# Kernel optimization log

Measured on AMD Instinct MI355X. Metric: run time of the kernel, lower is better.

The kernel has to match this reference:

```python
import jax, jax.numpy as jnp
import numpy as np

N, C, H = 8192, 512, 8


def setup_inputs() -> dict:
    key = jax.random.key(0)
    ks = jax.random.split(key, 5)
    s = 1.0 / np.sqrt(C)
    return {
        "x": jax.random.normal(ks[0], (N, C), dtype=jnp.float32),
        "W_theta": jax.random.normal(ks[1], (C, C), dtype=jnp.float32) * s,
        "b_theta": jnp.zeros((C,), dtype=jnp.float32),
        "W_phi": jax.random.normal(ks[2], (C, C), dtype=jnp.float32) * s,
        "b_phi": jnp.zeros((C,), dtype=jnp.float32),
        "W_k": jax.random.normal(ks[3], (H, C, C), dtype=jnp.float32) * s,
        "b_k": jnp.zeros((H, C), dtype=jnp.float32),
    }


def reference(x, W_theta, b_theta, W_phi, b_phi, W_k, b_k):
    # query/key projections: (N, C)
    query = x @ W_theta + b_theta
    key = x @ W_phi + b_phi
    # dense N x N similarity + row softmax
    sim = query @ key.T                       # (N, N)
    adj = jax.nn.softmax(sim, axis=-1)        # (N, N)
    # per-head V projections, batched: (H, N, C)
    xk = jnp.einsum("nc,hcd->hnd", x, W_k) + b_k[:, None, :]
    # attention-weighted aggregation per head, relu, mean over heads
    out = jnp.einsum("nm,hmd->hnd", adj, xk)  # (H, N, C)
    return jax.nn.relu(out).mean(axis=0)      # (N, C)
```

## Files before the change

### kernel.cpp

```cpp
#include <hip/hip_runtime.h>
#include <hip/hip_bf16.h>
#include <cstdint>
#include <cstddef>

#define NN 8192
#define CC 512
#define HH 8

typedef __attribute__((ext_vector_type(8))) short short8;
typedef __attribute__((ext_vector_type(4))) float f32x4;

__device__ __forceinline__ void gload_lds16(const void* g, void* l) {
  __builtin_amdgcn_global_load_lds(
      (const __attribute__((address_space(1))) void*)g,
      (__attribute__((address_space(3))) void*)l, 16, 0, 0);
}

__device__ __forceinline__ f32x4 mfma16(short8 a, short8 b, f32x4 c) {
  return __builtin_amdgcn_mfma_f32_16x16x32_bf16(a, b, c, 0, 0, 0);
}

__device__ __forceinline__ float b2f(unsigned u) {
  union { unsigned i; float f; } x; x.i = u << 16; return x.f;
}

__device__ __forceinline__ void unpack8(uint4 v, float* f) {
  f[0] = b2f(v.x & 0xffffu); f[1] = b2f(v.x >> 16);
  f[2] = b2f(v.y & 0xffffu); f[3] = b2f(v.y >> 16);
  f[4] = b2f(v.z & 0xffffu); f[5] = b2f(v.z >> 16);
  f[6] = b2f(v.w & 0xffffu); f[7] = b2f(v.w >> 16);
}

__global__ __launch_bounds__(256, 2) void gemm_qk(
    const __hip_bfloat16* __restrict__ ah, const __hip_bfloat16* __restrict__ al, int lda,
    const __hip_bfloat16* __restrict__ bh, const __hip_bfloat16* __restrict__ bl, int ldb,
    int K,
    __hip_bfloat16* __restrict__ outHi, __hip_bfloat16* __restrict__ outLo, int ldc,
    const float* __restrict__ biasCol)
{
  __shared__ __align__(16) char lds[32768];
  const int tid  = threadIdx.x;
  const int lane = tid & 63;
  const int wave = tid >> 6;
  const int bm = blockIdx.y, bn = blockIdx.x;
  const int wr = wave >> 1, wc = wave & 1;
  const int fr = lane & 15, fq = lane >> 4;

  f32x4 acc[4][4] = {};

  for (int kt = 0; kt < K; kt += 32) {
    __syncthreads();
#pragma unroll
    for (int tile = 0; tile < 4; ++tile) {
      const __hip_bfloat16* tp = (tile == 0) ? ah : (tile == 1) ? al
                               : (tile == 2) ? bh : bl;
      const int ld = (tile < 2) ? lda : ldb;
      const int tb = ((tile < 2) ? bm : bn) * 128;
#pragma unroll
      for (int half = 0; half < 2; ++half) {
        int sub = half * 256 + tid;
        int row = sub >> 2, ch = sub & 3;
        gload_lds16(tp + (size_t)(tb + row) * ld + kt + ch * 8,
                    lds + tile * 8192 + sub * 16);
      }
    }
    __syncthreads();

    short8 fah[4], fal[4], fbh[4], fbl[4];
#pragma unroll
    for (int i = 0; i < 4; ++i) {
      const int ra = (wr * 64 + i * 16 + fr) * 64 + fq * 16;
      const int rb = (wc * 64 + i * 16 + fr) * 64 + fq * 16;
      fah[i] = *(const short8*)(lds +         ra);
      fal[i] = *(const short8*)(lds +  8192 + ra);
      fbh[i] = *(const short8*)(lds + 16384 + rb);
      fbl[i] = *(const short8*)(lds + 24576 + rb);
    }
#pragma unroll
    for (int i = 0; i < 4; ++i)
#pragma unroll
      for (int j = 0; j < 4; ++j) {
        acc[i][j] = mfma16(fah[i], fbh[j], acc[i][j]);
        acc[i][j] = mfma16(fah[i], fbl[j], acc[i][j]);
        acc[i][j] = mfma16(fal[i], fbh[j], acc[i][j]);
      }
  }

#pragma unroll
  for (int i = 0; i < 4; ++i)
#pragma unroll
    for (int j = 0; j < 4; ++j) {
      const int rbase = bm * 128 + wr * 64 + i * 16 + fq * 4;
      const int col   = bn * 128 + wc * 64 + j * 16 + fr;
#pragma unroll
      for (int t = 0; t < 4; ++t) {
        float v = acc[i][j][t] + biasCol[col];
        __hip_bfloat16 h = __float2bfloat16(v);
        outHi[(size_t)(rbase + t) * ldc + col] = h;
        outLo[(size_t)(rbase + t) * ldc + col] = __float2bfloat16(v - __bfloat162float(h));
      }
    }
}

__global__ __launch_bounds__(512, 2) void gemm_sim(
    const __hip_bfloat16* __restrict__ A, int lda,
    const __hip_bfloat16* __restrict__ B, int ldb,
    int K,
    float* __restrict__ segMax, unsigned char* __restrict__ sim4)
{
  (void)K;
  __shared__ __align__(16) char lds[98304];
  const int tid  = threadIdx.x;
  const int lane = tid & 63;
  const int wave = tid >> 6;
  const int bm = blockIdx.y, bn = blockIdx.x;
  const int wm = wave >> 2;
  const int wn = wave & 3;
  const int fr = lane & 15, fq = lane >> 4;

  int s0 = tid * 16;          s0 ^= ((s0 >> 9) & 1) << 5;
  int s1 = 8192 + tid * 16;   s1 ^= ((s1 >> 9) & 1) << 5;
  const int off0 = (s0 >> 6) * 1024 + ((s0 & 63) >> 1);
  const int off1 = (s1 >> 6) * 1024 + ((s1 & 63) >> 1);

  const int fl = ((fr >> 3) & 1) << 5;
  const int baseAs = (((wm * 128 + fr) * 64) + fq * 16) ^ fl;
  const int baseBs = (((wn * 64 + fr) * 64) + fq * 16) ^ fl;

  const __hip_bfloat16* Ab = A + (size_t)bm * 256 * lda;
  const __hip_bfloat16* Bb = B + (size_t)bn * 256 * ldb;

#define STAGE_C0(t, buf) do {                                                \
    const __hip_bfloat16* ap_ = Ab + (t) * 32;                               \
    const __hip_bfloat16* bp_ = Bb + (t) * 32;                               \
    gload_lds16(ap_ + off0, lds + (buf) * 16384 + tid * 16);                 \
    gload_lds16(bp_ + off0, lds + 49152 + (buf) * 16384 + tid * 16);         \
  } while (0)
#define STAGE_C1(t, buf) do {                                                \
    const __hip_bfloat16* ap_ = Ab + (t) * 32;                               \
    const __hip_bfloat16* bp_ = Bb + (t) * 32;                               \
    gload_lds16(ap_ + off1, lds + (buf) * 16384 + 8192 + tid * 16);          \
    gload_lds16(bp_ + off1, lds + 49152 + (buf) * 16384 + 8192 + tid * 16);  \
  } while (0)

  f32x4 acc[8][4] = {};

  STAGE_C0(0, 0); STAGE_C1(0, 0);
  STAGE_C0(1, 1); STAGE_C1(1, 1);

#pragma unroll
  for (int t = 0; t < 16; ++t) {
    const int buf = t % 3;
    const int nbuf = (t + 2) % 3;
    const char* Abuf = lds + buf * 16384;
    const char* Bbuf = lds + 49152 + buf * 16384;

    if (t == 15) asm volatile("s_waitcnt vmcnt(0)" ::: "memory");
    else         asm volatile("s_waitcnt vmcnt(4)" ::: "memory");
    __builtin_amdgcn_s_barrier();
    __builtin_amdgcn_sched_barrier(0);

    short8 a[8], b4[4];
#pragma unroll
    for (int i = 0; i < 4; ++i)
      a[i] = *(const short8*)(Abuf + baseAs + i * 1024);
#pragma unroll
    for (int j = 0; j < 4; ++j)
      b4[j] = *(const short8*)(Bbuf + baseBs + j * 1024);
    if (t < 14) STAGE_C0(t + 2, nbuf);

#pragma unroll
    for (int i = 0; i < 4; ++i)
#pragma unroll
      for (int j = 0; j < 4; ++j)
        acc[i][j] = mfma16(a[i], b4[j], acc[i][j]);

#pragma unroll
    for (int i = 0; i < 4; ++i)
      a[4 + i] = *(const short8*)(Abuf + baseAs + (4 + i) * 1024);
    if (t < 14) STAGE_C1(t + 2, nbuf);

#pragma unroll
    for (int i = 0; i < 4; ++i)
#pragma unroll
      for (int j = 0; j < 4; ++j)
        acc[4 + i][j] = mfma16(a[4 + i], b4[j], acc[4 + i][j]);
  }
#undef STAGE_C0
#undef STAGE_C1

  const int seg = bn * 4 + wn;
#pragma unroll
  for (int i = 0; i < 8; ++i)
#pragma unroll
    for (int tt = 0; tt < 4; ++tt) {
      const int row = bm * 256 + wm * 128 + i * 16 + fq * 4 + tt;
      float mx = fmaxf(fmaxf(acc[i][0][tt], acc[i][1][tt]),
                       fmaxf(acc[i][2][tt], acc[i][3][tt]));
      mx = fmaxf(mx, __shfl_xor(mx, 1));
      mx = fmaxf(mx, __shfl_xor(mx, 2));
      mx = fmaxf(mx, __shfl_xor(mx, 4));
      mx = fmaxf(mx, __shfl_xor(mx, 8));
      if (fr == 0) segMax[(size_t)row * 128 + seg] = mx;
      unsigned q[4];
#pragma unroll
      for (int j = 0; j < 4; ++j)
        q[j] = (unsigned)fminf((mx - acc[i][j][tt]) * (4.0f / 3.0f), 15.0f);
      unsigned char* dst = sim4 + (size_t)row * (NN / 2) + seg * 32 + fr;
      dst[0]  = (unsigned char)(q[0] | (q[1] << 4));
      dst[16] = (unsigned char)(q[2] | (q[3] << 4));
    }
}

__global__ __launch_bounds__(256) void select_zgather(
    const float* __restrict__ segMax, const unsigned char* __restrict__ sim4,
    const __hip_bfloat16* __restrict__ QKhi, const __hip_bfloat16* __restrict__ QKlo,
    const float* __restrict__ x,
    __hip_bfloat16* __restrict__ z)
{
  const int lane = threadIdx.x & 63;
  const int n = blockIdx.x * 4 + (threadIdx.x >> 6);

  float2 sm = ((const float2*)(segMax + (size_t)n * 128))[lane];
  float M = fmaxf(sm.x, sm.y);
#pragma unroll
  for (int off = 32; off; off >>= 1) M = fmaxf(M, __shfl_xor(M, off));

  const unsigned long long b0 = __ballot(sm.x > M - 11.0f);
  const unsigned long long b1 = __ballot(sm.y > M - 11.0f);

  float qf[8];
  {
    uint4 qh4 = ((const uint4*)(QKhi + (size_t)n * 1024))[lane];
    uint4 ql4 = ((const uint4*)(QKlo + (size_t)n * 1024))[lane];
    float a[8], b[8];
    unpack8(qh4, a); unpack8(ql4, b);
#pragma unroll
    for (int e = 0; e < 8; ++e) qf[e] = a[e] + b[e];
  }

  const unsigned char* srow4 = sim4 + (size_t)n * (NN / 2);
  const int jj = lane >> 4;
  const int shift = (jj & 1) * 4;
  const int boff = (jj >> 1) * 16 + (lane & 15);

  int nk = 0;
  float se_mine = -1e30f;
  int   mm_mine = 0;
#pragma unroll
  for (int half = 0; half < 2; ++half) {
    unsigned long long mask = half ? b1 : b0;
    while (mask) {
      const int b = __ffsll((unsigned long long)mask) - 1;
      mask &= mask - 1;
      const int seg = 2 * b + half;
      const float segv = __shfl(half ? sm.y : sm.x, b);
      const unsigned byte = srow4[seg * 32 + boff];
      const float sa = segv - 0.75f * (float)((byte >> shift) & 15u);
      unsigned long long cm = __ballot(sa > M - 11.0f);
      while (cm) {
        const int c = __ffsll((unsigned long long)cm) - 1;
        cm &= cm - 1;
        const int m = seg * 64 + c;
        uint4 kh4 = ((const uint4*)(QKhi + (size_t)m * 1024 + 512))[lane];
        uint4 kl4 = ((const uint4*)(QKlo + (size_t)m * 1024 + 512))[lane];
        float a[8], bb[8];
        unpack8(kh4, a); unpack8(kl4, bb);
        float p = 0.f;
#pragma unroll
        for (int e = 0; e < 8; ++e) p += qf[e] * (a[e] + bb[e]);
#pragma unroll
        for (int off = 32; off; off >>= 1) p += __shfl_xor(p, off);
        if (p > M - 10.5f) {
          if (lane == nk) { se_mine = p; mm_mine = m; }
          nk = (nk < 63) ? nk + 1 : nk;
        }
      }
    }
  }

  float Me = (lane < nk) ? se_mine : -1e30f;
#pragma unroll
  for (int off = 32; off; off >>= 1) Me = fmaxf(Me, __shfl_xor(Me, off));
  const float wv = __expf(se_mine - Me);
  float Lr = (lane < nk) ? wv : 0.f;
#pragma unroll
  for (int off = 32; off; off >>= 1) Lr += __shfl_xor(Lr, off);

  float acc[8] = {};
  for (int i = 0; i < nk; ++i) {
    const int   m = __shfl(mm_mine, i);
    const float w = __shfl(wv, i);
    const float4* row = (const float4*)(x + (size_t)m * CC + 8 * lane);
    float4 a = row[0], b = row[1];
    acc[0] += w * a.x; acc[1] += w * a.y; acc[2] += w * a.z; acc[3] += w * a.w;
    acc[4] += w * b.x; acc[5] += w * b.y; acc[6] += w * b.z; acc[7] += w * b.w;
  }
  const float inv = 1.0f / Lr;
  short8 o;
#pragma unroll
  for (int e = 0; e < 8; ++e) {
    __hip_bfloat16 h = __float2bfloat16(acc[e] * inv);
    o[e] = *(short*)&h;
  }
  *(short8*)(z + (size_t)n * CC + 8 * lane) = o;
}

__global__ __launch_bounds__(256, 2) void gemm_zwk(
    const __hip_bfloat16* __restrict__ z,
    const __hip_bfloat16* __restrict__ WkT,
    const float* __restrict__ bk,
    float* __restrict__ out)
{
  __shared__ __align__(16) char lds[16384];
  const int tid  = threadIdx.x;
  const int lane = tid & 63;
  const int wave = tid >> 6;
  const int bn = blockIdx.x, bm = blockIdx.y, hg = blockIdx.z;
  const int wr = wave >> 1, wc = wave & 1;
  const int fr = lane & 15, fq = lane >> 4;

  f32x4 oacc[4][4] = {};

  for (int hh = 0; hh < 4; ++hh) {
    const int head = hg * 4 + hh;
    const __hip_bfloat16* B = WkT + (size_t)(head * 512 + bn * 128) * CC;
    f32x4 acc[4][4] = {};
    for (int kt = 0; kt < CC; kt += 32) {
      __syncthreads();
#pragma unroll
      for (int half = 0; half < 2; ++half) {
        int sub = half * 256 + tid;
        int row = sub >> 2, ch = sub & 3;
        gload_lds16(z + (size_t)(bm * 128 + row) * CC + kt + ch * 8, lds +        sub * 16);
        gload_lds16(B + (size_t)row * CC + kt + ch * 8,              lds + 8192 + sub * 16);
      }
      __syncthreads();

      short8 af[4], bf[4];
#pragma unroll
      for (int i = 0; i < 4; ++i) {
        af[i] = *(const short8*)(lds +        (wr * 64 + i * 16 + fr) * 64 + fq * 16);
        bf[i] = *(const short8*)(lds + 8192 + (wc * 64 + i * 16 + fr) * 64 + fq * 16);
      }
#pragma unroll
      for (int i = 0; i < 4; ++i)
#pragma unroll
        for (int j = 0; j < 4; ++j)
          acc[i][j] = mfma16(af[i], bf[j], acc[i][j]);
    }
#pragma unroll
    for (int j = 0; j < 4; ++j) {
      const int d = bn * 128 + wc * 64 + j * 16 + fr;
      const float bias = bk[head * CC + d];
#pragma unroll
      for (int i = 0; i < 4; ++i)
#pragma unroll
        for (int t = 0; t < 4; ++t)
          oacc[i][j][t] += fmaxf(acc[i][j][t] + bias, 0.f);
    }
  }

#pragma unroll
  for (int i = 0; i < 4; ++i)
#pragma unroll
    for (int j = 0; j < 4; ++j) {
      const int rbase = bm * 128 + wr * 64 + i * 16 + fq * 4;
      const int d     = bn * 128 + wc * 64 + j * 16 + fr;
#pragma unroll
      for (int t = 0; t < 4; ++t)
        atomicAdd(out + (size_t)(rbase + t) * CC + d, 0.125f * oacc[i][j][t]);
    }
}

__global__ void prep_all(const float* __restrict__ x,
                         const float* __restrict__ Wth, const float* __restrict__ Wph,
                         const float* __restrict__ bt, const float* __restrict__ bp,
                         const float* __restrict__ Wk,
                         __hip_bfloat16* __restrict__ xhi, __hip_bfloat16* __restrict__ xlo,
                         __hip_bfloat16* __restrict__ wthi, __hip_bfloat16* __restrict__ wtlo,
                         __hip_bfloat16* __restrict__ wkt, float* __restrict__ biasqk,
                         float* __restrict__ outz) {
  int idx = blockIdx.x * 256 + threadIdx.x;
  if (idx < 4194304) {
    float v = x[idx];
    __hip_bfloat16 h = __float2bfloat16(v);
    xhi[idx] = h;
    xlo[idx] = __float2bfloat16(v - __bfloat162float(h));
  } else if (idx < 4718592) {
    int i = idx - 4194304;
    int j = i >> 9, c = i & 511;
    const float* W = (j < 512) ? Wth : Wph;
    float v = W[(size_t)c * 512 + (j & 511)];
    __hip_bfloat16 h = __float2bfloat16(v);
    wthi[i] = h;
    wtlo[i] = __float2bfloat16(v - __bfloat162float(h));
  } else if (idx < 6815744) {
    int i = idx - 4718592;
    int j = i >> 9, c = i & 511;
    float v = Wk[(size_t)(j >> 9) * 262144 + (size_t)c * 512 + (j & 511)];
    wkt[i] = __float2bfloat16(v);
  } else if (idx < 6816768) {
    int i = idx - 6815744;
    biasqk[i] = (i < 512) ? bt[i] : bp[i - 512];
  } else if (idx < 7865344) {
    int i = idx - 6816768;
    ((float4*)outz)[i] = make_float4(0.f, 0.f, 0.f, 0.f);
  }
}

extern "C" void kernel_launch(void* const* d_in, const int* in_sizes, int n_in,
                              void* d_out, int out_size, void* d_ws, size_t ws_size,
                              hipStream_t stream) {
  const float* x  = (const float*)d_in[0];
  const float* Wt = (const float*)d_in[1];
  const float* bt = (const float*)d_in[2];
  const float* Wp = (const float*)d_in[3];
  const float* bp = (const float*)d_in[4];
  const float* Wk = (const float*)d_in[5];
  const float* bk = (const float*)d_in[6];
  float* out = (float*)d_out;

  const size_t MB = 1024 * 1024;
  char* w = (char*)d_ws;
  __hip_bfloat16* xhi  = (__hip_bfloat16*)(w + 0 * MB);
  __hip_bfloat16* xlo  = (__hip_bfloat16*)(w + 8 * MB);
  __hip_bfloat16* WThi = (__hip_bfloat16*)(w + 16 * MB);
  __hip_bfloat16* WTlo = (__hip_bfloat16*)(w + 17 * MB);
  float*          biasqk = (float*)(w + 18 * MB);
  __hip_bfloat16* WkT  = (__hip_bfloat16*)(w + 20 * MB);
  __hip_bfloat16* QKhi = (__hip_bfloat16*)(w + 24 * MB);
  __hip_bfloat16* QKlo = (__hip_bfloat16*)(w + 40 * MB);
  __hip_bfloat16* z    = (__hip_bfloat16*)(w + 56 * MB);
  float*          segMax = (float*)(w + 64 * MB);
  unsigned char*  sim4   = (unsigned char*)(w + 68 * MB);

  prep_all<<<7865344 / 256, 256, 0, stream>>>(x, Wt, Wp, bt, bp, Wk,
                                              xhi, xlo, WThi, WTlo, WkT, biasqk,
                                              out);

  gemm_qk<<<dim3(1024 / 128, NN / 128), 256, 0, stream>>>(
      xhi, xlo, CC, WThi, WTlo, CC, CC, QKhi, QKlo, 1024, biasqk);

  gemm_sim<<<dim3(NN / 256, NN / 256), 512, 0, stream>>>(
      QKhi, 1024, QKhi + 512, 1024, CC, segMax, sim4);

  select_zgather<<<NN / 4, 256, 0, stream>>>(segMax, sim4, QKhi, QKlo, x, z);

  gemm_zwk<<<dim3(CC / 128, NN / 128, 2), 256, 0, stream>>>(z, WkT, bk, out);
}
```

Before: 315.1 us.

## Triple-buffer LDS staging in gemm_zwk with XOR swizzle and one barrier per step

Rewrites the z×WkT GEMM mainloop to use a three-stage LDS ring. Global-to-LDS loads are issued two k-steps ahead across head boundaries, and each step waits with s_waitcnt vmcnt plus a single barrier instead of two syncthreads. Adds an XOR swizzle on the LDS layout to cut bank conflicts on fragment reads. LDS use grows from 16KB to 48KB per block, which may reduce occupancy under launch_bounds(256,2). The full unroll of 64 k-steps also increases code size.

```diff
diff --git a/kernel.cpp b/kernel.cpp
--- a/kernel.cpp
+++ b/kernel.cpp
@@ -312,7 +312,7 @@
     const float* __restrict__ bk,
     float* __restrict__ out)
 {
-  __shared__ __align__(16) char lds[16384];
+  __shared__ __align__(16) char lds[49152];
   const int tid  = threadIdx.x;
   const int lane = tid & 63;
   const int wave = tid >> 6;
@@ -320,35 +320,63 @@
   const int wr = wave >> 1, wc = wave & 1;
   const int fr = lane & 15, fq = lane >> 4;
 
+  int s0 = tid * 16;         s0 ^= ((s0 >> 9) & 1) << 5;
+  int s1 = 4096 + tid * 16;  s1 ^= ((s1 >> 9) & 1) << 5;
+  const int r0 = s0 >> 6, c0 = (s0 & 63) >> 1;
+  const int r1 = s1 >> 6, c1 = (s1 & 63) >> 1;
+
+  const int fl = ((fr >> 3) & 1) << 5;
+  const int baseA = (((wr * 64 + fr) * 64) + fq * 16) ^ fl;
+  const int baseB = (((wc * 64 + fr) * 64) + fq * 16) ^ fl;
+
+  const __hip_bfloat16* zb = z + (size_t)(bm * 128) * CC;
+
+#define STAGE_VT(vt, buf) do {                                               \
+    const int h_ = hg * 4 + ((vt) >> 4);                                     \
+    const int k_ = ((vt) & 15) * 32;                                         \
+    const __hip_bfloat16* Bp_ = WkT + (size_t)(h_ * 512 + bn * 128) * CC;    \
+    gload_lds16(zb  + (size_t)r0 * CC + k_ + c0, lds + (buf) * 16384 + tid * 16);        \
+    gload_lds16(zb  + (size_t)r1 * CC + k_ + c1, lds + (buf) * 16384 + 4096 + tid * 16); \
+    gload_lds16(Bp_ + (size_t)r0 * CC + k_ + c0, lds + (buf) * 16384 + 8192 + tid * 16); \
+    gload_lds16(Bp_ + (size_t)r1 * CC + k_ + c1, lds + (buf) * 16384 + 12288 + tid * 16);\
+  } while (0)
+
   f32x4 oacc[4][4] = {};
 
+  STAGE_VT(0, 0);
+  STAGE_VT(1, 1);
+
+#pragma unroll
   for (int hh = 0; hh < 4; ++hh) {
-    const int head = hg * 4 + hh;
-    const __hip_bfloat16* B = WkT + (size_t)(head * 512 + bn * 128) * CC;
     f32x4 acc[4][4] = {};
-    for (int kt = 0; kt < CC; kt += 32) {
-      __syncthreads();
-#pragma unroll
-      for (int half = 0; half < 2; ++half) {
-        int sub = half * 256 + tid;
-        int row = sub >> 2, ch = sub & 3;
-        gload_lds16(z + (size_t)(bm * 128 + row) * CC + kt + ch * 8, lds +        sub * 16);
-        gload_lds16(B + (size_t)row * CC + kt + ch * 8,              lds + 8192 + sub * 16);
+#pragma unroll
+    for (int k2 = 0; k2 < 16; ++k2) {
+      const int vt = hh * 16 + k2;
+      const int buf = vt % 3;
+      const char* Abuf = lds + buf * 16384;
+      const char* Bbuf = lds + buf * 16384 + 8192;
+
+      if (vt == 63) asm volatile("s_waitcnt vmcnt(0)" ::: "memory");
+      else          asm volatile("s_waitcnt vmcnt(4)" ::: "memory");
+      __builtin_amdgcn_s_barrier();
+      __builtin_amdgcn_sched_barrier(0);
+
+      short8 af[4], bf[4];
+#pragma unroll
+      for (int i = 0; i < 4; ++i) {
+        af[i] = *(const short8*)(Abuf + baseA + i * 1024);
+        bf[i] = *(const short8*)(Bbuf + baseB + i * 1024);
       }
-      __syncthreads();
-
-      short8 af[4], bf[4];
-#pragma unroll
-      for (int i = 0; i < 4; ++i) {
-        af[i] = *(const short8*)(lds +        (wr * 64 + i * 16 + fr) * 64 + fq * 16);
-        bf[i] = *(const short8*)(lds + 8192 + (wc * 64 + i * 16 + fr) * 64 + fq * 16);
-      }
+      if (vt < 62) STAGE_VT(vt + 2, (vt + 2) % 3);
+
 #pragma unroll
       for (int i = 0; i < 4; ++i)
 #pragma unroll
         for (int j = 0; j < 4; ++j)
           acc[i][j] = mfma16(af[i], bf[j], acc[i][j]);
     }
+
+    const int head = hg * 4 + hh;
 #pragma unroll
     for (int j = 0; j < 4; ++j) {
       const int d = bn * 128 + wc * 64 + j * 16 + fr;
@@ -360,6 +388,7 @@
           oacc[i][j][t] += fmaxf(acc[i][j][t] + bias, 0.f);
     }
   }
+#undef STAGE_VT
 
 #pragma unroll
   for (int i = 0; i < 4; ++i)
```

Result: no change. 314.5 us (-0.2%).
